# Optimization experiments

Hardware: AMD Instinct MI355X
Metric: run time of the kernel (lower is better)

The kernel has to match this reference:

```python
import jax, jax.numpy as jnp
import numpy as np

SEQ_LEN, BATCH, HID = 2048, 16, 512  # hidden last dim is 2*HID (bi-directional)
N_SPANS = 200000
EPS = 1e-12


def setup_inputs() -> dict:
    key = jax.random.key(0)
    k1, k2, k3, k4, k5, k6, k7 = jax.random.split(key, 7)
    hidden = jax.random.normal(k1, (SEQ_LEN, BATCH, 2 * HID), dtype=jnp.float32)
    bids = jax.random.randint(k2, (N_SPANS,), 0, BATCH, dtype=jnp.int32)
    begins = jax.random.randint(k3, (N_SPANS,), 1, SEQ_LEN, dtype=jnp.int32)  # begin-1 >= 0
    ends = jax.random.randint(k4, (N_SPANS,), 0, SEQ_LEN, dtype=jnp.int32)
    targets = jax.random.bernoulli(k5, 0.5, (N_SPANS,)).astype(jnp.float32)
    W = jax.random.normal(k6, (2 * HID, 1), dtype=jnp.float32) * (1.0 / np.sqrt(2 * HID))
    b = jax.random.normal(k7, (1,), dtype=jnp.float32) * 0.01
    return {"hidden": hidden, "bids": bids, "begins": begins, "ends": ends,
            "targets": targets, "W": W, "b": b}


def reference(hidden, bids, begins, ends, targets, W, b):
    # span feature: cat(hidden[begin-1, bid, :H], hidden[end, bid, H:])  -> [N, 2H]
    fwd = hidden[begins - 1, bids, :HID]   # forward-direction state at begin-1
    bwd = hidden[ends, bids, HID:]         # backward-direction state at end
    feats = jnp.concatenate([fwd, bwd], axis=-1)        # [N, 2H]
    logits = feats @ W + b                               # [N, 1]
    p = jax.nn.sigmoid(logits)[:, 0]                     # [N]
    t = targets
    # F.binary_cross_entropy (mean reduction); dropout inactive in eval
    bce = -(t * jnp.log(jnp.clip(p, EPS, 1.0)) + (1.0 - t) * jnp.log(jnp.clip(1.0 - p, EPS, 1.0)))
    return jnp.mean(bce)
```

## Files before the change

### kernel.cpp

```cpp
#include <hip/hip_runtime.h>


#define HIDD 512
#define FEAT 1024
#define NROWS (2048 * 16)
#define NWAVES_PER_BLOCK 4

__device__ __forceinline__ float dot4(float4 a, float4 w) {
    return a.x * w.x + a.y * w.y + a.z * w.z + a.w * w.w;
}

__global__ __launch_bounds__(256) void row_dot_kernel(
    const float* __restrict__ hidden,
    const float* __restrict__ W,
    float*       __restrict__ tab,
    int nrows)
{
    const int lane  = threadIdx.x & 63;
    const int wid   = threadIdx.x >> 6;
    const int gwave = blockIdx.x * NWAVES_PER_BLOCK + wid;
    const int nwaves = gridDim.x * NWAVES_PER_BLOCK;

    const float4* W4 = reinterpret_cast<const float4*>(W);
    const float4 w0 = W4[lane];
    const float4 w1 = W4[64 + lane];
    const float4 w2 = W4[128 + lane];
    const float4 w3 = W4[192 + lane];

    for (int row = gwave; row < nrows; row += nwaves) {
        const float4* r = reinterpret_cast<const float4*>(hidden + (size_t)row * FEAT);
        const float4 a0 = r[lane];
        const float4 a1 = r[64 + lane];
        const float4 a2 = r[128 + lane];
        const float4 a3 = r[192 + lane];

        float df = dot4(a0, w0) + dot4(a1, w1);
        float db = dot4(a2, w2) + dot4(a3, w3);

        #pragma unroll
        for (int off = 32; off >= 1; off >>= 1) {
            df += __shfl_xor(df, off, 64);
            db += __shfl_xor(db, off, 64);
        }
        if (lane == 0) {
            tab[row] = df;
            tab[nrows + row] = db;
        }
    }
}

__global__ __launch_bounds__(256) void span_bce_kernel(
    const float* __restrict__ tab,
    const int*   __restrict__ bids,
    const int*   __restrict__ begins,
    const int*   __restrict__ ends,
    const float* __restrict__ targets,
    const float* __restrict__ bias_p,
    float*       __restrict__ out,
    int nspans, float inv_n, int nrows)
{
    const float bias = bias_p[0];
    float acc = 0.0f;

    for (int i = blockIdx.x * blockDim.x + threadIdx.x; i < nspans;
         i += gridDim.x * blockDim.x) {
        const int   bid = bids[i];
        const int   fr  = (begins[i] - 1) * 16 + bid;
        const int   br  = ends[i] * 16 + bid;
        const float t   = targets[i];

        const float z  = tab[fr] + tab[nrows + br] + bias;
        const float p  = 1.0f / (1.0f + expf(-z));
        const float pc = fminf(fmaxf(p, 1e-12f), 1.0f);
        const float qc = fminf(fmaxf(1.0f - p, 1e-12f), 1.0f);
        acc += -(t * logf(pc) + (1.0f - t) * logf(qc));
    }

    #pragma unroll
    for (int off = 32; off >= 1; off >>= 1)
        acc += __shfl_xor(acc, off, 64);

    __shared__ float sacc[NWAVES_PER_BLOCK];
    const int lane = threadIdx.x & 63;
    const int wid  = threadIdx.x >> 6;
    if (lane == 0) sacc[wid] = acc;
    __syncthreads();
    if (threadIdx.x == 0) {
        float s = 0.0f;
        #pragma unroll
        for (int i = 0; i < NWAVES_PER_BLOCK; ++i) s += sacc[i];
        atomicAdd(out, s * inv_n);
    }
}

__global__ __launch_bounds__(256) void phrase_cls_fallback(
    const float* __restrict__ hidden,
    const int*   __restrict__ bids,
    const int*   __restrict__ begins,
    const int*   __restrict__ ends,
    const float* __restrict__ targets,
    const float* __restrict__ W,
    const float* __restrict__ bias_p,
    float*       __restrict__ out,
    int nspans, float inv_n)
{
    const int lane  = threadIdx.x & 63;
    const int wid   = threadIdx.x >> 6;
    const int gwave = blockIdx.x * NWAVES_PER_BLOCK + wid;
    const int nwaves = gridDim.x * NWAVES_PER_BLOCK;

    const float4* W4 = reinterpret_cast<const float4*>(W);
    const float4 w0 = W4[lane];
    const float4 w1 = W4[64 + lane];
    const float4 w2 = W4[128 + lane];
    const float4 w3 = W4[192 + lane];
    const float bias = bias_p[0];

    float acc = 0.0f;
    for (int s = gwave; s < nspans; s += nwaves) {
        const int   bid = bids[s];
        const int   beg = begins[s] - 1;
        const int   end = ends[s];
        const float t   = targets[s];
        const float4* frow = reinterpret_cast<const float4*>(
            hidden + ((size_t)beg * 16 + (size_t)bid) * FEAT);
        const float4* brow = reinterpret_cast<const float4*>(
            hidden + ((size_t)end * 16 + (size_t)bid) * FEAT + HIDD);
        float d = dot4(frow[lane], w0) + dot4(frow[64 + lane], w1)
                + dot4(brow[lane], w2) + dot4(brow[64 + lane], w3);
        #pragma unroll
        for (int off = 32; off >= 1; off >>= 1)
            d += __shfl_xor(d, off, 64);
        if (lane == 0) {
            const float z  = d + bias;
            const float p  = 1.0f / (1.0f + expf(-z));
            const float pc = fminf(fmaxf(p, 1e-12f), 1.0f);
            const float qc = fminf(fmaxf(1.0f - p, 1e-12f), 1.0f);
            acc += -(t * logf(pc) + (1.0f - t) * logf(qc));
        }
    }
    __shared__ float sacc[NWAVES_PER_BLOCK];
    if (lane == 0) sacc[wid] = acc;
    __syncthreads();
    if (threadIdx.x == 0) {
        float s = 0.0f;
        #pragma unroll
        for (int i = 0; i < NWAVES_PER_BLOCK; ++i) s += sacc[i];
        atomicAdd(out, s * inv_n);
    }
}

extern "C" void kernel_launch(void* const* d_in, const int* in_sizes, int n_in,
                              void* d_out, int out_size, void* d_ws, size_t ws_size,
                              hipStream_t stream) {
    const float* hidden  = (const float*)d_in[0];
    const int*   bids    = (const int*)  d_in[1];
    const int*   begins  = (const int*)  d_in[2];
    const int*   ends    = (const int*)  d_in[3];
    const float* targets = (const float*)d_in[4];
    const float* W       = (const float*)d_in[5];
    const float* b       = (const float*)d_in[6];
    float* out = (float*)d_out;

    const int nspans = in_sizes[1];
    const float inv_n = 1.0f / (float)nspans;

    hipMemsetAsync(out, 0, sizeof(float), stream);

    const size_t tab_bytes = (size_t)2 * NROWS * sizeof(float);
    if (ws_size >= tab_bytes) {
        float* tab = (float*)d_ws;
        row_dot_kernel<<<4096, 256, 0, stream>>>(hidden, W, tab, NROWS);
        const int blocks2 = (nspans + 255) / 256;
        span_bce_kernel<<<blocks2, 256, 0, stream>>>(
            tab, bids, begins, ends, targets, b, out, nspans, inv_n, NROWS);
    } else {
        phrase_cls_fallback<<<2048, 256, 0, stream>>>(
            hidden, bids, begins, ends, targets, W, b, out, nspans, inv_n);
    }
}
```

Measured before the change: 214.2 us.

## Process two rows per wave and replace atomics with two-stage deterministic reduction

The row-dot kernel now handles two adjacent rows per wave iteration with half the grid, putting more loads in flight per wave. The span kernel writes per-block partial sums to workspace instead of doing an atomicAdd on the output. A single-block final kernel then reduces the partials and writes the mean, which also removes the memset. This trades one extra kernel launch for no atomic contention, and gives a deterministic sum order.

Result: no change. 210.1 us (-1.9%).

```diff
diff --git a/kernel.cpp b/kernel.cpp
--- a/kernel.cpp
+++ b/kernel.cpp
@@ -5,9 +5,17 @@
 #define FEAT 1024
 #define NROWS (2048 * 16)
 #define NWAVES_PER_BLOCK 4
+#define K2_BLOCK 256
 
 __device__ __forceinline__ float dot4(float4 a, float4 w) {
     return a.x * w.x + a.y * w.y + a.z * w.z + a.w * w.w;
+}
+
+__device__ __forceinline__ float wave_reduce(float v) {
+    #pragma unroll
+    for (int off = 32; off >= 1; off >>= 1)
+        v += __shfl_xor(v, off, 64);
+    return v;
 }
 
 __global__ __launch_bounds__(256) void row_dot_kernel(
@@ -27,43 +35,53 @@
     const float4 w2 = W4[128 + lane];
     const float4 w3 = W4[192 + lane];
 
-    for (int row = gwave; row < nrows; row += nwaves) {
-        const float4* r = reinterpret_cast<const float4*>(hidden + (size_t)row * FEAT);
-        const float4 a0 = r[lane];
-        const float4 a1 = r[64 + lane];
-        const float4 a2 = r[128 + lane];
-        const float4 a3 = r[192 + lane];
-
-        float df = dot4(a0, w0) + dot4(a1, w1);
-        float db = dot4(a2, w2) + dot4(a3, w3);
-
-        #pragma unroll
-        for (int off = 32; off >= 1; off >>= 1) {
-            df += __shfl_xor(df, off, 64);
-            db += __shfl_xor(db, off, 64);
+    for (int row = gwave * 2; row < nrows; row += nwaves * 2) {
+        const float4* r0 = reinterpret_cast<const float4*>(hidden + (size_t)row * FEAT);
+        const float4* r1 = reinterpret_cast<const float4*>(hidden + (size_t)(row + 1) * FEAT);
+
+        const float4 a0 = r0[lane];
+        const float4 a1 = r0[64 + lane];
+        const float4 a2 = r0[128 + lane];
+        const float4 a3 = r0[192 + lane];
+        const float4 b0 = r1[lane];
+        const float4 b1 = r1[64 + lane];
+        const float4 b2 = r1[128 + lane];
+        const float4 b3 = r1[192 + lane];
+
+        float df0 = dot4(a0, w0) + dot4(a1, w1);
+        float db0 = dot4(a2, w2) + dot4(a3, w3);
+        float df1 = dot4(b0, w0) + dot4(b1, w1);
+        float db1 = dot4(b2, w2) + dot4(b3, w3);
+
+        df0 = wave_reduce(df0);
+        db0 = wave_reduce(db0);
+        df1 = wave_reduce(df1);
+        db1 = wave_reduce(db1);
+
+        if (lane == 0) {
+            tab[row]             = df0;
+            tab[row + 1]         = df1;
+            tab[nrows + row]     = db0;
+            tab[nrows + row + 1] = db1;
         }
-        if (lane == 0) {
-            tab[row] = df;
-            tab[nrows + row] = db;
-        }
-    }
-}
-
-__global__ __launch_bounds__(256) void span_bce_kernel(
+    }
+}
+
+__global__ __launch_bounds__(K2_BLOCK) void span_bce_kernel(
     const float* __restrict__ tab,
     const int*   __restrict__ bids,
     const int*   __restrict__ begins,
     const int*   __restrict__ ends,
     const float* __restrict__ targets,
     const float* __restrict__ bias_p,
-    float*       __restrict__ out,
-    int nspans, float inv_n, int nrows)
+    float*       __restrict__ partials,
+    int nspans, int nrows)
 {
     const float bias = bias_p[0];
     float acc = 0.0f;
 
-    for (int i = blockIdx.x * blockDim.x + threadIdx.x; i < nspans;
-         i += gridDim.x * blockDim.x) {
+    const int i = blockIdx.x * K2_BLOCK + threadIdx.x;
+    if (i < nspans) {
         const int   bid = bids[i];
         const int   fr  = (begins[i] - 1) * 16 + bid;
         const int   br  = ends[i] * 16 + bid;
@@ -73,14 +91,12 @@
         const float p  = 1.0f / (1.0f + expf(-z));
         const float pc = fminf(fmaxf(p, 1e-12f), 1.0f);
         const float qc = fminf(fmaxf(1.0f - p, 1e-12f), 1.0f);
-        acc += -(t * logf(pc) + (1.0f - t) * logf(qc));
-    }
-
-    #pragma unroll
-    for (int off = 32; off >= 1; off >>= 1)
-        acc += __shfl_xor(acc, off, 64);
-
-    __shared__ float sacc[NWAVES_PER_BLOCK];
+        acc = -(t * logf(pc) + (1.0f - t) * logf(qc));
+    }
+
+    acc = wave_reduce(acc);
+
+    __shared__ float sacc[K2_BLOCK / 64];
     const int lane = threadIdx.x & 63;
     const int wid  = threadIdx.x >> 6;
     if (lane == 0) sacc[wid] = acc;
@@ -88,9 +104,28 @@
     if (threadIdx.x == 0) {
         float s = 0.0f;
         #pragma unroll
-        for (int i = 0; i < NWAVES_PER_BLOCK; ++i) s += sacc[i];
-        atomicAdd(out, s * inv_n);
-    }
+        for (int k = 0; k < K2_BLOCK / 64; ++k) s += sacc[k];
+        partials[blockIdx.x] = s;
+    }
+}
+
+__global__ __launch_bounds__(256) void final_reduce_kernel(
+    const float* __restrict__ partials,
+    float*       __restrict__ out,
+    int n, float inv_n)
+{
+    float acc = 0.0f;
+    for (int i = threadIdx.x; i < n; i += 256)
+        acc += partials[i];
+    acc = wave_reduce(acc);
+
+    __shared__ float sacc[4];
+    const int lane = threadIdx.x & 63;
+    const int wid  = threadIdx.x >> 6;
+    if (lane == 0) sacc[wid] = acc;
+    __syncthreads();
+    if (threadIdx.x == 0)
+        out[0] = (sacc[0] + sacc[1] + sacc[2] + sacc[3]) * inv_n;
 }
 
 __global__ __launch_bounds__(256) void phrase_cls_fallback(
@@ -128,9 +163,7 @@
             hidden + ((size_t)end * 16 + (size_t)bid) * FEAT + HIDD);
         float d = dot4(frow[lane], w0) + dot4(frow[64 + lane], w1)
                 + dot4(brow[lane], w2) + dot4(brow[64 + lane], w3);
-        #pragma unroll
-        for (int off = 32; off >= 1; off >>= 1)
-            d += __shfl_xor(d, off, 64);
+        d = wave_reduce(d);
         if (lane == 0) {
             const float z  = d + bias;
             const float p  = 1.0f / (1.0f + expf(-z));
@@ -164,17 +197,18 @@
 
     const int nspans = in_sizes[1];
     const float inv_n = 1.0f / (float)nspans;
-
-    hipMemsetAsync(out, 0, sizeof(float), stream);
-
-    const size_t tab_bytes = (size_t)2 * NROWS * sizeof(float);
-    if (ws_size >= tab_bytes) {
-        float* tab = (float*)d_ws;
-        row_dot_kernel<<<4096, 256, 0, stream>>>(hidden, W, tab, NROWS);
-        const int blocks2 = (nspans + 255) / 256;
-        span_bce_kernel<<<blocks2, 256, 0, stream>>>(
-            tab, bids, begins, ends, targets, b, out, nspans, inv_n, NROWS);
+    const int blocks2 = (nspans + K2_BLOCK - 1) / K2_BLOCK;
+
+    const size_t need = ((size_t)2 * NROWS + (size_t)blocks2) * sizeof(float);
+    if (ws_size >= need) {
+        float* tab      = (float*)d_ws;
+        float* partials = tab + 2 * NROWS;
+        row_dot_kernel<<<2048, 256, 0, stream>>>(hidden, W, tab, NROWS);
+        span_bce_kernel<<<blocks2, K2_BLOCK, 0, stream>>>(
+            tab, bids, begins, ends, targets, b, partials, nspans, NROWS);
+        final_reduce_kernel<<<1, 256, 0, stream>>>(partials, out, blocks2, inv_n);
     } else {
+        hipMemsetAsync(out, 0, sizeof(float), stream);
         phrase_cls_fallback<<<2048, 256, 0, stream>>>(
             hidden, bids, begins, ends, targets, W, b, out, nspans, inv_n);
     }
```
